# Optimization experiments

Measured on AMD Instinct MI355X. Metric: run time of the kernel, lower is better.

## Reference

```python
import jax, jax.numpy as jnp
import numpy as np

B = 1024
IN_SIZE = 8192
OUT_SIZE = 8192
CONNECTIVITY = 32
NNZ = OUT_SIZE * CONNECTIVITY  # 262144


def setup_inputs() -> dict:
    key = jax.random.key(0)
    kx, kv, ki = jax.random.split(key, 3)
    x = jax.random.normal(kx, (B, IN_SIZE), dtype=jnp.float32)
    # uniform init as in module: (rand-0.5)*2*sqrt(3/connectivity)
    scale = np.sqrt(3.0 / CONNECTIVITY)
    values = (jax.random.uniform(kv, (NNZ,), dtype=jnp.float32) - 0.5) * 2.0 * scale
    # indices_out = list(range(out_size)) * connectivity -> arange(nnz) % out_size
    idx_out = (jnp.arange(NNZ) % OUT_SIZE).astype(jnp.int32)
    # uniform distribution: randperm(nnz) % in_size ~ uniform over [0, in_size)
    idx_in = jax.random.randint(ki, (NNZ,), 0, IN_SIZE, dtype=jnp.int32)
    return {"x": x, "values": values, "idx_out": idx_out, "idx_in": idx_in,
            "out_size": OUT_SIZE}


def reference(x, values, idx_out, idx_in, out_size):
    # y[b, o] = sum over nnz k with idx_out[k]==o of values[k] * x[b, idx_in[k]]
    # (spmm(indices, values, out, in, x.T).T in the original)
    contrib = x[:, idx_in] * values[None, :]          # [B, nnz]
    y = jnp.zeros((x.shape[0], out_size), dtype=x.dtype)
    y = y.at[:, idx_out].add(contrib)                 # scatter-add over output rows
    return y
```

## Files before the change

### kernel.cpp

```cpp
#include <hip/hip_runtime.h>

#define IN_SIZE   8192
#define OUT_SIZE  8192
#define CONN      32
#define NNZ       (OUT_SIZE * CONN)
#define BATCH     1024
#define BT        8
#define OT        4096
#define NTHREADS  1024
#define OPT       (OT / NTHREADS)

typedef int          int4v   __attribute__((ext_vector_type(4)));
typedef float        float2v __attribute__((ext_vector_type(2)));
typedef float        float4v __attribute__((ext_vector_type(4)));
typedef unsigned int uint4v  __attribute__((ext_vector_type(4)));

__device__ __forceinline__ unsigned bf16rne(float f) {
  unsigned u = __builtin_bit_cast(unsigned, f);
  return (u + 0x7fffu + ((u >> 16) & 1u)) >> 16;
}

__global__ __launch_bounds__(256)
void pack_kernel(const float* __restrict__ values,
                 const int*   __restrict__ idx_in,
                 unsigned int* __restrict__ pk) {
  int k = blockIdx.x * 256 + threadIdx.x;
  if (k < NNZ) {
    unsigned u = __builtin_bit_cast(unsigned, values[k]);
    unsigned r = (u + 0xFFFu + ((u >> 13) & 1u)) >> 13;
    unsigned i = (unsigned)idx_in[k];
    unsigned s = ((i & 3u) << 11) | (i >> 2);
    pk[k] = (s << 19) | (r & 0x7FFFFu);
  }
}

template<bool PACKED>
__global__ __launch_bounds__(NTHREADS, 4)
void spl_kernel(const float* __restrict__ x,
                const unsigned int* __restrict__ pk,
                const float* __restrict__ values,
                const int* __restrict__ idx_in,
                float* __restrict__ y) {
  __shared__ uint4v xs[IN_SIZE];

  const int bid = blockIdx.x;
  const int oh  = bid >> 7;
  const int bb  = bid & 127;
  const int b0  = bb * BT;
  const int t   = threadIdx.x;
  const int o0  = oh * OT + t * OPT;

  {
    float4v r[2][BT];
    #pragma unroll
    for (int p = 0; p < 2; ++p) {
      const int c4 = p * NTHREADS + t;
      #pragma unroll
      for (int b = 0; b < BT; ++b)
        r[p][b] = *(const float4v*)(x + (size_t)(b0 + b) * IN_SIZE + c4 * 4);
    }
    #pragma unroll
    for (int p = 0; p < 2; ++p) {
      const int c4 = p * NTHREADS + t;
      #pragma unroll
      for (int q = 0; q < 4; ++q) {
        uint4v w;
        w.x = bf16rne(r[p][0][q]) | (bf16rne(r[p][1][q]) << 16);
        w.y = bf16rne(r[p][2][q]) | (bf16rne(r[p][3][q]) << 16);
        w.z = bf16rne(r[p][4][q]) | (bf16rne(r[p][5][q]) << 16);
        w.w = bf16rne(r[p][6][q]) | (bf16rne(r[p][7][q]) << 16);
        xs[q * 2048 + c4] = w;
      }
    }
  }

  if constexpr (PACKED) {
    const char* xsb = (const char*)xs;

#define LDPK(J)  (*(const uint4v*)(pk + (J) * OUT_SIZE + o0))
#define GATHER(G, P)                                                        \
    {                                                                       \
      _Pragma("unroll")                                                     \
      for (int q = 0; q < OPT; ++q)                                         \
        G[q] = *(const uint4v*)(xsb + ((P[q] >> 15) & 0x1FFF0u));           \
    }
#define CONSUME(P, G)                                                       \
    {                                                                       \
      _Pragma("unroll")                                                     \
      for (int q = 0; q < OPT; ++q) {                                       \
        float v = __builtin_bit_cast(float, P[q] << 13);                    \
        float2v v2 = {v, v};                                                \
        _Pragma("unroll")                                                   \
        for (int c = 0; c < 4; ++c) {                                       \
          float2v xp = {__builtin_bit_cast(float, G[q][c] << 16),           \
                        __builtin_bit_cast(float, G[q][c] & 0xFFFF0000u)};  \
          acc2[q][c] += v2 * xp;                                            \
        }                                                                   \
      }                                                                     \
    }

    uint4v pk0 = LDPK(0);
    uint4v pk1 = LDPK(1);

    __syncthreads();

    float2v acc2[OPT][4];
    #pragma unroll
    for (int q = 0; q < OPT; ++q)
      #pragma unroll
      for (int c = 0; c < 4; ++c) acc2[q][c] = (float2v){0.0f, 0.0f};

    uint4v g0[OPT];
    GATHER(g0, pk0);

    #pragma unroll
    for (int j = 0; j < CONN; j += 2) {
      uint4v pk2 = LDPK(j + 2 < CONN ? j + 2 : 0);
      uint4v g1[OPT];
      GATHER(g1, pk1);
      CONSUME(pk0, g0);
      uint4v pk3 = LDPK(j + 3 < CONN ? j + 3 : 0);
      uint4v g2[OPT];
      GATHER(g2, pk2);
      CONSUME(pk1, g1);
      pk0 = pk2; pk1 = pk3;
      #pragma unroll
      for (int q = 0; q < OPT; ++q) g0[q] = g2[q];
    }
#undef LDPK
#undef GATHER
#undef CONSUME

    #pragma unroll
    for (int bt = 0; bt < BT; ++bt) {
      float* yr = y + (size_t)(b0 + bt) * OUT_SIZE + o0;
      const int c = bt >> 1, h = bt & 1;
      float4v w = {acc2[0][c][h], acc2[1][c][h], acc2[2][c][h], acc2[3][c][h]};
      __builtin_nontemporal_store(w, (float4v*)yr);
    }
  } else {
    __syncthreads();
    float acc[OPT][BT];
    #pragma unroll
    for (int q = 0; q < OPT; ++q)
      #pragma unroll
      for (int bt = 0; bt < BT; ++bt) acc[q][bt] = 0.0f;
    const char* xsb = (const char*)xs;
    for (int j = 0; j < CONN; ++j) {
      const int kb = j * OUT_SIZE + o0;
      int4v i0 = *(const int4v*)(idx_in + kb);
      float4v v0 = *(const float4v*)(values + kb);
      #pragma unroll
      for (int q = 0; q < OPT; ++q) {
        unsigned i = (unsigned)i0[q];
        unsigned s = ((i & 3u) << 11) | (i >> 2);
        float v = v0[q];
        uint4v gv = *(const uint4v*)(xsb + (s << 4));
        acc[q][0] += v * __builtin_bit_cast(float, gv.x << 16);
        acc[q][1] += v * __builtin_bit_cast(float, gv.x & 0xFFFF0000u);
        acc[q][2] += v * __builtin_bit_cast(float, gv.y << 16);
        acc[q][3] += v * __builtin_bit_cast(float, gv.y & 0xFFFF0000u);
        acc[q][4] += v * __builtin_bit_cast(float, gv.z << 16);
        acc[q][5] += v * __builtin_bit_cast(float, gv.z & 0xFFFF0000u);
        acc[q][6] += v * __builtin_bit_cast(float, gv.w << 16);
        acc[q][7] += v * __builtin_bit_cast(float, gv.w & 0xFFFF0000u);
      }
    }
    #pragma unroll
    for (int bt = 0; bt < BT; ++bt) {
      float* yr = y + (size_t)(b0 + bt) * OUT_SIZE + o0;
      float4v w = {acc[0][bt], acc[1][bt], acc[2][bt], acc[3][bt]};
      __builtin_nontemporal_store(w, (float4v*)yr);
    }
  }
}

extern "C" void kernel_launch(void* const* d_in, const int* in_sizes, int n_in,
                              void* d_out, int out_size, void* d_ws, size_t ws_size,
                              hipStream_t stream) {
  const float* x      = (const float*)d_in[0];
  const float* values = (const float*)d_in[1];
  const int*   idx_in = (const int*)d_in[3];
  float*       y      = (float*)d_out;

  const dim3 grid((BATCH / BT) * (OUT_SIZE / OT));
  const dim3 blk(NTHREADS);

  if (ws_size >= (size_t)NNZ * sizeof(unsigned int)) {
    unsigned int* pk = (unsigned int*)d_ws;
    hipLaunchKernelGGL(pack_kernel, dim3(NNZ / 256), dim3(256), 0, stream,
                       values, idx_in, pk);
    hipLaunchKernelGGL((spl_kernel<true>), grid, blk, 0, stream,
                       x, pk, values, idx_in, y);
  } else {
    hipLaunchKernelGGL((spl_kernel<false>), grid, blk, 0, stream,
                       x, nullptr, values, idx_in, y);
  }
}
```

Measured before the change: 32.99 us.

## Split per-thread outputs into two sequential passes with deeper index prefetch

Each thread now handles two pairs of outputs in two sequential passes (oA and oB halves) instead of four outputs at once. This halves the live accumulator and gather registers and lets the loop prefetch packed indices four steps ahead instead of two. The outputs of the first pass are written before the second pass starts, and the nontemporal stores become plain 8-byte and 16-byte stores. The trade-off is narrower pk loads and output stores, plus a second pipeline ramp-up per thread.

```diff
diff --git a/kernel.cpp b/kernel.cpp
--- a/kernel.cpp
+++ b/kernel.cpp
@@ -8,11 +8,12 @@
 #define BT        8
 #define OT        4096
 #define NTHREADS  1024
-#define OPT       (OT / NTHREADS)
+#define HALF_OT   2048
 
 typedef int          int4v   __attribute__((ext_vector_type(4)));
 typedef float        float2v __attribute__((ext_vector_type(2)));
 typedef float        float4v __attribute__((ext_vector_type(4)));
+typedef unsigned int uint2v  __attribute__((ext_vector_type(2)));
 typedef unsigned int uint4v  __attribute__((ext_vector_type(4)));
 
 __device__ __forceinline__ unsigned bf16rne(float f) {
@@ -48,7 +49,6 @@
   const int bb  = bid & 127;
   const int b0  = bb * BT;
   const int t   = threadIdx.x;
-  const int o0  = oh * OT + t * OPT;
 
   {
     float4v r[2][BT];
@@ -76,18 +76,19 @@
 
   if constexpr (PACKED) {
     const char* xsb = (const char*)xs;
-
-#define LDPK(J)  (*(const uint4v*)(pk + (J) * OUT_SIZE + o0))
-#define GATHER(G, P)                                                        \
+    const int oA = oh * OT + 2 * t;
+    const int oB = oA + HALF_OT;
+
+#define LDPK2(BASE, J)  (*(const uint2v*)(pk + (J) * OUT_SIZE + (BASE)))
+#define GATHER2(G, P)                                                       \
+    {                                                                       \
+      G[0] = *(const uint4v*)(xsb + ((P.x >> 15) & 0x1FFF0u));              \
+      G[1] = *(const uint4v*)(xsb + ((P.y >> 15) & 0x1FFF0u));              \
+    }
+#define CONSUME2(P, G)                                                      \
     {                                                                       \
       _Pragma("unroll")                                                     \
-      for (int q = 0; q < OPT; ++q)                                         \
-        G[q] = *(const uint4v*)(xsb + ((P[q] >> 15) & 0x1FFF0u));           \
-    }
-#define CONSUME(P, G)                                                       \
-    {                                                                       \
-      _Pragma("unroll")                                                     \
-      for (int q = 0; q < OPT; ++q) {                                       \
+      for (int q = 0; q < 2; ++q) {                                         \
         float v = __builtin_bit_cast(float, P[q] << 13);                    \
         float2v v2 = {v, v};                                                \
         _Pragma("unroll")                                                   \
@@ -98,51 +99,78 @@
         }                                                                   \
       }                                                                     \
     }
-
-    uint4v pk0 = LDPK(0);
-    uint4v pk1 = LDPK(1);
+#define PASS_LOOP(BASE)                                                     \
+    {                                                                       \
+      uint4v g0[2], g1[2];                                                  \
+      GATHER2(g0, pk0);                                                     \
+      GATHER2(g1, pk1);                                                     \
+      _Pragma("unroll")                                                     \
+      for (int j = 0; j < CONN; j += 2) {                                   \
+        uint2v pk4 = LDPK2(BASE, j + 4 < CONN ? j + 4 : 0);                 \
+        uint4v g2[2];                                                       \
+        GATHER2(g2, pk2);                                                   \
+        CONSUME2(pk0, g0);                                                  \
+        uint2v pk5 = LDPK2(BASE, j + 5 < CONN ? j + 5 : 0);                 \
+        uint4v g3[2];                                                       \
+        GATHER2(g3, pk3);                                                   \
+        CONSUME2(pk1, g1);                                                  \
+        pk0 = pk2; pk1 = pk3; pk2 = pk4; pk3 = pk5;                         \
+        _Pragma("unroll")                                                   \
+        for (int q = 0; q < 2; ++q) { g0[q] = g2[q]; g1[q] = g3[q]; }       \
+      }                                                                     \
+    }
+
+    uint2v pk0 = LDPK2(oA, 0);
+    uint2v pk1 = LDPK2(oA, 1);
+    uint2v pk2 = LDPK2(oA, 2);
+    uint2v pk3 = LDPK2(oA, 3);
 
     __syncthreads();
 
-    float2v acc2[OPT][4];
-    #pragma unroll
-    for (int q = 0; q < OPT; ++q)
+    float2v acc2[2][4];
+    #pragma unroll
+    for (int q = 0; q < 2; ++q)
       #pragma unroll
       for (int c = 0; c < 4; ++c) acc2[q][c] = (float2v){0.0f, 0.0f};
 
-    uint4v g0[OPT];
-    GATHER(g0, pk0);
-
-    #pragma unroll
-    for (int j = 0; j < CONN; j += 2) {
-      uint4v pk2 = LDPK(j + 2 < CONN ? j + 2 : 0);
-      uint4v g1[OPT];
-      GATHER(g1, pk1);
-      CONSUME(pk0, g0);
-      uint4v pk3 = LDPK(j + 3 < CONN ? j + 3 : 0);
-      uint4v g2[OPT];
-      GATHER(g2, pk2);
-      CONSUME(pk1, g1);
-      pk0 = pk2; pk1 = pk3;
-      #pragma unroll
-      for (int q = 0; q < OPT; ++q) g0[q] = g2[q];
-    }
-#undef LDPK
-#undef GATHER
-#undef CONSUME
+    PASS_LOOP(oA);
+
+    uint2v pkB0 = LDPK2(oB, 0);
+    uint2v pkB1 = LDPK2(oB, 1);
+    uint2v pkB2 = LDPK2(oB, 2);
+    uint2v pkB3 = LDPK2(oB, 3);
 
     #pragma unroll
     for (int bt = 0; bt < BT; ++bt) {
-      float* yr = y + (size_t)(b0 + bt) * OUT_SIZE + o0;
       const int c = bt >> 1, h = bt & 1;
-      float4v w = {acc2[0][c][h], acc2[1][c][h], acc2[2][c][h], acc2[3][c][h]};
-      __builtin_nontemporal_store(w, (float4v*)yr);
-    }
+      float2v w = {acc2[0][c][h], acc2[1][c][h]};
+      *(float2v*)(y + (size_t)(b0 + bt) * OUT_SIZE + oA) = w;
+    }
+
+    pk0 = pkB0; pk1 = pkB1; pk2 = pkB2; pk3 = pkB3;
+    #pragma unroll
+    for (int q = 0; q < 2; ++q)
+      #pragma unroll
+      for (int c = 0; c < 4; ++c) acc2[q][c] = (float2v){0.0f, 0.0f};
+
+    PASS_LOOP(oB);
+
+    #pragma unroll
+    for (int bt = 0; bt < BT; ++bt) {
+      const int c = bt >> 1, h = bt & 1;
+      float2v w = {acc2[0][c][h], acc2[1][c][h]};
+      *(float2v*)(y + (size_t)(b0 + bt) * OUT_SIZE + oB) = w;
+    }
+#undef LDPK2
+#undef GATHER2
+#undef CONSUME2
+#undef PASS_LOOP
   } else {
     __syncthreads();
-    float acc[OPT][BT];
-    #pragma unroll
-    for (int q = 0; q < OPT; ++q)
+    const int o0 = oh * OT + t * 4;
+    float acc[4][BT];
+    #pragma unroll
+    for (int q = 0; q < 4; ++q)
       #pragma unroll
       for (int bt = 0; bt < BT; ++bt) acc[q][bt] = 0.0f;
     const char* xsb = (const char*)xs;
@@ -151,7 +179,7 @@
       int4v i0 = *(const int4v*)(idx_in + kb);
       float4v v0 = *(const float4v*)(values + kb);
       #pragma unroll
-      for (int q = 0; q < OPT; ++q) {
+      for (int q = 0; q < 4; ++q) {
         unsigned i = (unsigned)i0[q];
         unsigned s = ((i & 3u) << 11) | (i >> 2);
         float v = v0[q];
@@ -170,7 +198,7 @@
     for (int bt = 0; bt < BT; ++bt) {
       float* yr = y + (size_t)(b0 + bt) * OUT_SIZE + o0;
       float4v w = {acc[0][bt], acc[1][bt], acc[2][bt], acc[3][bt]};
-      __builtin_nontemporal_store(w, (float4v*)yr);
+      *(float4v*)yr = w;
     }
   }
 }
```

Result: slower. 36.37 us (+10.2%).
